# Kernel optimization log

Measured on AMD Instinct MI355X. Metric: run time of the kernel, lower is better.

The kernel has to match this reference:

```python
import jax, jax.numpy as jnp
import numpy as np

HEAD_DIM = 64  # hidden_dim 1024 // heads_num 16


def setup_inputs() -> dict:
    key = jax.random.key(0)
    ks = jax.random.split(key, 5)
    B, S, H = 2, 4096, 1024
    std = 1.0 / np.sqrt(H)
    return {
        "x": jax.random.normal(ks[0], (B, S, H), jnp.float32),
        "Wq": jax.random.normal(ks[1], (H, H), jnp.float32) * std,
        "bq": jnp.zeros((H,), jnp.float32),
        "Wk": jax.random.normal(ks[2], (H, H), jnp.float32) * std,
        "bk": jnp.zeros((H,), jnp.float32),
        "Wv": jax.random.normal(ks[3], (H, H), jnp.float32) * std,
        "bv": jnp.zeros((H,), jnp.float32),
        "Wo": jax.random.normal(ks[4], (H, H), jnp.float32) * std,
        "bo": jnp.zeros((H,), jnp.float32),
    }


def reference(x, Wq, bq, Wk, bk, Wv, bv, Wo, bo):
    # Linear projections (torch Linear: x @ W^T + b)
    q = jnp.einsum("bsh,oh->bso", x, Wq) + bq
    k = jnp.einsum("bsh,oh->bso", x, Wk) + bk
    v = jnp.einsum("bsh,oh->bso", x, Wv) + bv
    # all_to_all is identity on a single device (world size 1)
    scale = jnp.float32(HEAD_DIM) ** 0.5
    # Faithful to source: attention over the FULL hidden dim (no head split),
    # full [B, S, S] score matrix.
    scores = jnp.einsum("bqh,bkh->bqk", q, k) / scale
    weights = jax.nn.softmax(scores, axis=-1)
    attn = jnp.einsum("bqk,bkh->bqh", weights, v)
    out = jnp.einsum("bsh,oh->bso", attn, Wo) + bo
    return out
```

## Files before the change

### kernel.cpp

```cpp
#include <hip/hip_runtime.h>
#include <stdint.h>


typedef __bf16 bf16x8 __attribute__((ext_vector_type(8)));
typedef float  f32x4  __attribute__((ext_vector_type(4)));

__device__ __forceinline__ unsigned short f32_to_bf16_rne(float f) {
    uint32_t u = __builtin_bit_cast(uint32_t, f);
    uint32_t r = (u + 0x7FFFu + ((u >> 16) & 1u)) >> 16;
    return (unsigned short)r;
}

__global__ __launch_bounds__(256) void cvt_f32_bf16(
    const float* __restrict__ x, unsigned short* __restrict__ y, int n)
{
    int i = (blockIdx.x * 256 + threadIdx.x) * 4;
    if (i < n) {
        float4 v = *(const float4*)(x + i);
        ushort4 o;
        o.x = f32_to_bf16_rne(v.x);
        o.y = f32_to_bf16_rne(v.y);
        o.z = f32_to_bf16_rne(v.z);
        o.w = f32_to_bf16_rne(v.w);
        *(ushort4*)(y + i) = o;
    }
}

__global__ __launch_bounds__(256) void cvt_weights(
    const float* __restrict__ w0, const float* __restrict__ w1,
    const float* __restrict__ w2, const float* __restrict__ w3,
    unsigned short* __restrict__ dst, float* __restrict__ rsum)
{
    int b = blockIdx.x;
    if (b >= 4096) {
        int i = ((b - 4096) * 256 + threadIdx.x) * 4;
        *(float4*)(rsum + i) = float4{0.f, 0.f, 0.f, 0.f};
        return;
    }
    int which = b >> 10;
    const float* src = which == 0 ? w0 : which == 1 ? w1 : which == 2 ? w2 : w3;
    int i = ((b & 1023) * 256 + threadIdx.x) * 4;
    float4 v = *(const float4*)(src + i);
    ushort4 o;
    o.x = f32_to_bf16_rne(v.x);
    o.y = f32_to_bf16_rne(v.y);
    o.z = f32_to_bf16_rne(v.z);
    o.w = f32_to_bf16_rne(v.w);
    *(ushort4*)(dst + (size_t)which * 1048576 + i) = o;
}

#define BM 128
#define BN 128
#define BK 64

template <int MODE>
__global__ __launch_bounds__(256) void gemm_bt(
    const unsigned short* __restrict__ A,
    const unsigned short* __restrict__ Bt,
    void* __restrict__ C, void* __restrict__ C2,
    const float* __restrict__ b0, const float* __restrict__ b1,
    const float* __restrict__ b2, float* __restrict__ rowsum,
    float alpha, int M, int N, int K,
    long long aZ, long long bZ, long long cZ)
{
    __shared__ unsigned short ldsA[BM * BK];
    __shared__ unsigned short ldsB[BN * BK];

    int G  = gridDim.x * gridDim.y * gridDim.z;
    int l  = blockIdx.x + gridDim.x * (blockIdx.y + gridDim.y * blockIdx.z);
    int mb, nb, zb;
    if ((G & 7) == 0) {
        int perx = G >> 3;
        int idx  = (l & 7) * perx + (l >> 3);
        int NB = gridDim.x, Z = gridDim.z;
        mb = idx / (NB * Z);
        int rem = idx - mb * (NB * Z);
        zb = rem / NB;
        nb = rem - zb * NB;
    } else {
        mb = blockIdx.y; nb = blockIdx.x; zb = blockIdx.z;
    }

    const unsigned short* Ab = A  + (size_t)zb * aZ;
    const unsigned short* Bb = Bt + (size_t)zb * bZ;

    const int tid  = threadIdx.x;
    const int lane = tid & 63;
    const int wave = tid >> 6;
    const int quad = lane >> 4;
    const int l16  = lane & 15;
    const int wr   = wave >> 1;
    const int wc   = wave & 1;

    const int mBase = mb * BM;
    const int nBase = nb * BN;

    f32x4 acc[4][4] = {};

    for (int k0 = 0; k0 < K; k0 += BK) {
        #pragma unroll
        for (int i = 0; i < 4; ++i) {
            int base = (i * 4 + wave) * 64;
            int s    = base + lane;
            int row  = s >> 3;
            int col  = ((s ^ (s >> 3)) & 7) * 8;
            __builtin_amdgcn_global_load_lds(
                (const __attribute__((address_space(1))) void*)(Ab + (size_t)(mBase + row) * K + (size_t)(k0 + col)),
                (__attribute__((address_space(3))) void*)(&ldsA[base * 8]),
                16, 0, 0);
        }
        #pragma unroll
        for (int i = 0; i < 4; ++i) {
            int base = (i * 4 + wave) * 64;
            int s    = base + lane;
            int row  = s >> 3;
            int col  = ((s ^ (s >> 3)) & 7) * 8;
            __builtin_amdgcn_global_load_lds(
                (const __attribute__((address_space(1))) void*)(Bb + (size_t)(nBase + row) * K + (size_t)(k0 + col)),
                (__attribute__((address_space(3))) void*)(&ldsB[base * 8]),
                16, 0, 0);
        }
        __syncthreads();

        #pragma unroll
        for (int kk = 0; kk < 2; ++kk) {
            bf16x8 af[4], bfv[4];
            #pragma unroll
            for (int mi = 0; mi < 4; ++mi) {
                int r = wr * 64 + mi * 16 + l16;
                int c = kk * 4 + quad;
                af[mi] = *(const bf16x8*)(&ldsA[r * BK + (((c ^ r) & 7) << 3)]);
            }
            #pragma unroll
            for (int ni = 0; ni < 4; ++ni) {
                int r = wc * 64 + ni * 16 + l16;
                int c = kk * 4 + quad;
                bfv[ni] = *(const bf16x8*)(&ldsB[r * BK + (((c ^ r) & 7) << 3)]);
            }
            #pragma unroll
            for (int mi = 0; mi < 4; ++mi)
                #pragma unroll
                for (int ni = 0; ni < 4; ++ni)
                    acc[mi][ni] = __builtin_amdgcn_mfma_f32_16x16x32_bf16(
                        af[mi], bfv[ni], acc[mi][ni], 0, 0, 0);
        }
        __syncthreads();
    }

    if (MODE == 1) {
        unsigned short* Cz = (unsigned short*)C + (size_t)zb * cZ;
        #pragma unroll
        for (int mi = 0; mi < 4; ++mi)
            #pragma unroll
            for (int ni = 0; ni < 4; ++ni) {
                int col = nBase + wc * 64 + ni * 16 + l16;
                float b = b0 ? b0[col] : 0.f;
                #pragma unroll
                for (int r = 0; r < 4; ++r) {
                    int row = mBase + wr * 64 + mi * 16 + quad * 4 + r;
                    Cz[(size_t)row * N + col] = f32_to_bf16_rne(acc[mi][ni][r] + b);
                }
            }
    } else if (MODE == 3) {
        unsigned short* Pz = (unsigned short*)C + (size_t)zb * cZ;
        float* rs = rowsum + (size_t)zb * M;
        #pragma unroll
        for (int mi = 0; mi < 4; ++mi) {
            #pragma unroll
            for (int r = 0; r < 4; ++r) {
                int row = mBase + wr * 64 + mi * 16 + quad * 4 + r;
                float e[4];
                float partial = 0.f;
                #pragma unroll
                for (int ni = 0; ni < 4; ++ni) {
                    e[ni] = __expf(acc[mi][ni][r] * alpha);
                    partial += e[ni];
                }
                #pragma unroll
                for (int ni = 0; ni < 4; ++ni) {
                    int col = nBase + wc * 64 + ni * 16 + l16;
                    Pz[(size_t)row * N + col] = f32_to_bf16_rne(e[ni]);
                }
                #pragma unroll
                for (int off = 1; off < 16; off <<= 1)
                    partial += __shfl_xor(partial, off, 64);
                if (l16 == 0) atomicAdd(&rs[row], partial);
            }
        }
    } else if (MODE == 5) {
        const float* bias = (zb == 0) ? b0 : (zb == 1) ? b1 : b2;
        unsigned short* Cz = (zb < 2) ? ((unsigned short*)C + (size_t)zb * cZ)
                                      : (unsigned short*)C2;
        #pragma unroll
        for (int mi = 0; mi < 4; ++mi)
            #pragma unroll
            for (int ni = 0; ni < 4; ++ni) {
                int col = nBase + wc * 64 + ni * 16 + l16;
                float b = bias[col];
                #pragma unroll
                for (int r = 0; r < 4; ++r) {
                    int row = mBase + wr * 64 + mi * 16 + quad * 4 + r;
                    Cz[(size_t)row * N + col] = f32_to_bf16_rne(acc[mi][ni][r] + b);
                }
            }
    } else {
        float* Cz = (float*)C + (size_t)zb * cZ;
        const float* rs = rowsum + (size_t)zb * M;
        #pragma unroll
        for (int mi = 0; mi < 4; ++mi) {
            #pragma unroll
            for (int r = 0; r < 4; ++r) {
                int row = mBase + wr * 64 + mi * 16 + quad * 4 + r;
                float inv = 1.f / rs[row];
                #pragma unroll
                for (int ni = 0; ni < 4; ++ni) {
                    int col = nBase + wc * 64 + ni * 16 + l16;
                    Cz[(size_t)row * N + col] = acc[mi][ni][r] * inv + b0[col];
                }
            }
        }
    }
}

extern "C" void kernel_launch(void* const* d_in, const int* in_sizes, int n_in,
                              void* d_out, int out_size, void* d_ws, size_t ws_size,
                              hipStream_t stream)
{
    const float* x  = (const float*)d_in[0];
    const float* Wq = (const float*)d_in[1];
    const float* bq = (const float*)d_in[2];
    const float* Wk = (const float*)d_in[3];
    const float* bk = (const float*)d_in[4];
    const float* Wv = (const float*)d_in[5];
    const float* bv = (const float*)d_in[6];
    const float* Wo = (const float*)d_in[7];
    const float* bo = (const float*)d_in[8];
    float* out = (float*)d_out;

    const int Bsz = 2, S = 4096, H = 1024;
    const int M = Bsz * S;

    char* p = (char*)d_ws;
    auto alloc = [&](size_t bytes) -> char* {
        char* r = p; p += (bytes + 255) & ~(size_t)255; return r;
    };
    unsigned short* w16  = (unsigned short*)alloc((size_t)4 * H * H * 2);
    unsigned short* wq16 = w16;
    unsigned short* wo16 = w16 + (size_t)3 * H * H;
    unsigned short* q16  = (unsigned short*)alloc((size_t)M * H * 2);
    unsigned short* k16  = (unsigned short*)alloc((size_t)M * H * 2);
    unsigned short* vot16= (unsigned short*)alloc((size_t)Bsz * H * S * 2);
    float*          rsum = (float*)alloc((size_t)Bsz * S * 4);
    char* region = alloc((size_t)Bsz * S * S * 2);
    unsigned short* x16 = (unsigned short*)region;
    unsigned short* v16 = (unsigned short*)region + (size_t)M * H;
    unsigned short* p16 = (unsigned short*)region;

    cvt_f32_bf16<<<(M * H) / 1024, 256, 0, stream>>>(x, x16, M * H);
    cvt_weights<<<4096 + 8, 256, 0, stream>>>(Wq, Wk, Wv, Wo, w16, rsum);

    dim3 blk(256);

    gemm_bt<5><<<dim3(H / BN, M / BM, 3), blk, 0, stream>>>(
        x16, wq16, q16, v16, bq, bk, bv, nullptr, 1.f, M, H, H,
        0, (long long)H * H, (long long)M * H);

    gemm_bt<1><<<dim3(S / BN, H / BM, 2), blk, 0, stream>>>(
        wo16, v16, vot16, nullptr, nullptr, nullptr, nullptr, nullptr, 1.f,
        H, S, H, 0, (long long)S * H, (long long)H * S);

    gemm_bt<3><<<dim3(S / BN, S / BM, 2), blk, 0, stream>>>(
        q16, k16, p16, nullptr, nullptr, nullptr, nullptr, rsum, 0.125f,
        S, S, H, (long long)S * H, (long long)S * H, (long long)S * S);

    gemm_bt<6><<<dim3(H / BN, S / BM, 2), blk, 0, stream>>>(
        p16, vot16, out, nullptr, bo, nullptr, nullptr, rsum, 1.f,
        S, H, S, (long long)S * S, (long long)H * S, (long long)S * H);
}
```

Measured before the change: 387.0 us.

## Merge conversion kernels and fuse Wo·V and QK^T GEMMs into one launch

After: 386.0 us. No clear change (-0.3%).

```diff
diff --git a/kernel.cpp b/kernel.cpp
--- a/kernel.cpp
+++ b/kernel.cpp
@@ -11,75 +11,129 @@
     return (unsigned short)r;
 }
 
-__global__ __launch_bounds__(256) void cvt_f32_bf16(
-    const float* __restrict__ x, unsigned short* __restrict__ y, int n)
-{
-    int i = (blockIdx.x * 256 + threadIdx.x) * 4;
-    if (i < n) {
+#define BM 128
+#define BN 128
+#define BK 64
+
+__global__ __launch_bounds__(256) void cvt_all(
+    const float* __restrict__ x,
+    const float* __restrict__ w0, const float* __restrict__ w1,
+    const float* __restrict__ w2, const float* __restrict__ w3,
+    unsigned short* __restrict__ x16, unsigned short* __restrict__ w16,
+    float* __restrict__ rsum)
+{
+    int b = blockIdx.x;
+    if (b < 8192) {
+        int i = (b * 256 + threadIdx.x) * 4;
         float4 v = *(const float4*)(x + i);
         ushort4 o;
         o.x = f32_to_bf16_rne(v.x);
         o.y = f32_to_bf16_rne(v.y);
         o.z = f32_to_bf16_rne(v.z);
         o.w = f32_to_bf16_rne(v.w);
-        *(ushort4*)(y + i) = o;
-    }
-}
-
-__global__ __launch_bounds__(256) void cvt_weights(
-    const float* __restrict__ w0, const float* __restrict__ w1,
-    const float* __restrict__ w2, const float* __restrict__ w3,
-    unsigned short* __restrict__ dst, float* __restrict__ rsum)
-{
-    int b = blockIdx.x;
-    if (b >= 4096) {
-        int i = ((b - 4096) * 256 + threadIdx.x) * 4;
+        *(ushort4*)(x16 + i) = o;
+    } else if (b < 8192 + 4096) {
+        int bb = b - 8192;
+        int which = bb >> 10;
+        const float* src = which == 0 ? w0 : which == 1 ? w1 : which == 2 ? w2 : w3;
+        int i = ((bb & 1023) * 256 + threadIdx.x) * 4;
+        float4 v = *(const float4*)(src + i);
+        ushort4 o;
+        o.x = f32_to_bf16_rne(v.x);
+        o.y = f32_to_bf16_rne(v.y);
+        o.z = f32_to_bf16_rne(v.z);
+        o.w = f32_to_bf16_rne(v.w);
+        *(ushort4*)(w16 + (size_t)which * 1048576 + i) = o;
+    } else {
+        int i = ((b - 8192 - 4096) * 256 + threadIdx.x) * 4;
         *(float4*)(rsum + i) = float4{0.f, 0.f, 0.f, 0.f};
-        return;
-    }
-    int which = b >> 10;
-    const float* src = which == 0 ? w0 : which == 1 ? w1 : which == 2 ? w2 : w3;
-    int i = ((b & 1023) * 256 + threadIdx.x) * 4;
-    float4 v = *(const float4*)(src + i);
-    ushort4 o;
-    o.x = f32_to_bf16_rne(v.x);
-    o.y = f32_to_bf16_rne(v.y);
-    o.z = f32_to_bf16_rne(v.z);
-    o.w = f32_to_bf16_rne(v.w);
-    *(ushort4*)(dst + (size_t)which * 1048576 + i) = o;
-}
-
-#define BM 128
-#define BN 128
-#define BK 64
-
-template <int MODE>
+    }
+}
+
+template <int KC>
+__device__ __forceinline__ void gemm_core(
+    const unsigned short* __restrict__ Ab,
+    const unsigned short* __restrict__ Bb,
+    unsigned short* ldsA, unsigned short* ldsB,
+    int mBase, int nBase, int lane, int wave, f32x4 (&acc)[4][4])
+{
+    const int quad = lane >> 4;
+    const int l16  = lane & 15;
+    const int wr   = wave >> 1;
+    const int wc   = wave & 1;
+
+    for (int k0 = 0; k0 < KC; k0 += BK) {
+        #pragma unroll
+        for (int i = 0; i < 4; ++i) {
+            int base = (i * 4 + wave) * 64;
+            int s    = base + lane;
+            int row  = s >> 3;
+            int col  = ((s ^ (s >> 3)) & 7) * 8;
+            __builtin_amdgcn_global_load_lds(
+                (const __attribute__((address_space(1))) void*)(Ab + (size_t)(mBase + row) * KC + (size_t)(k0 + col)),
+                (__attribute__((address_space(3))) void*)(&ldsA[base * 8]),
+                16, 0, 0);
+        }
+        #pragma unroll
+        for (int i = 0; i < 4; ++i) {
+            int base = (i * 4 + wave) * 64;
+            int s    = base + lane;
+            int row  = s >> 3;
+            int col  = ((s ^ (s >> 3)) & 7) * 8;
+            __builtin_amdgcn_global_load_lds(
+                (const __attribute__((address_space(1))) void*)(Bb + (size_t)(nBase + row) * KC + (size_t)(k0 + col)),
+                (__attribute__((address_space(3))) void*)(&ldsB[base * 8]),
+                16, 0, 0);
+        }
+        __syncthreads();
+
+        #pragma unroll
+        for (int kk = 0; kk < 2; ++kk) {
+            bf16x8 af[4], bfv[4];
+            #pragma unroll
+            for (int mi = 0; mi < 4; ++mi) {
+                int r = wr * 64 + mi * 16 + l16;
+                int c = kk * 4 + quad;
+                af[mi] = *(const bf16x8*)(&ldsA[r * BK + (((c ^ r) & 7) << 3)]);
+            }
+            #pragma unroll
+            for (int ni = 0; ni < 4; ++ni) {
+                int r = wc * 64 + ni * 16 + l16;
+                int c = kk * 4 + quad;
+                bfv[ni] = *(const bf16x8*)(&ldsB[r * BK + (((c ^ r) & 7) << 3)]);
+            }
+            #pragma unroll
+            for (int mi = 0; mi < 4; ++mi)
+                #pragma unroll
+                for (int ni = 0; ni < 4; ++ni)
+                    acc[mi][ni] = __builtin_amdgcn_mfma_f32_16x16x32_bf16(
+                        af[mi], bfv[ni], acc[mi][ni], 0, 0, 0);
+        }
+        __syncthreads();
+    }
+}
+
+template <int MODE, int KC>
 __global__ __launch_bounds__(256) void gemm_bt(
     const unsigned short* __restrict__ A,
     const unsigned short* __restrict__ Bt,
     void* __restrict__ C, void* __restrict__ C2,
     const float* __restrict__ b0, const float* __restrict__ b1,
-    const float* __restrict__ b2, float* __restrict__ rowsum,
-    float alpha, int M, int N, int K,
-    long long aZ, long long bZ, long long cZ)
+    const float* __restrict__ b2, const float* __restrict__ rowsum,
+    int M, int N, long long aZ, long long bZ, long long cZ)
 {
     __shared__ unsigned short ldsA[BM * BK];
     __shared__ unsigned short ldsB[BN * BK];
 
     int G  = gridDim.x * gridDim.y * gridDim.z;
     int l  = blockIdx.x + gridDim.x * (blockIdx.y + gridDim.y * blockIdx.z);
-    int mb, nb, zb;
-    if ((G & 7) == 0) {
-        int perx = G >> 3;
-        int idx  = (l & 7) * perx + (l >> 3);
-        int NB = gridDim.x, Z = gridDim.z;
-        mb = idx / (NB * Z);
-        int rem = idx - mb * (NB * Z);
-        zb = rem / NB;
-        nb = rem - zb * NB;
-    } else {
-        mb = blockIdx.y; nb = blockIdx.x; zb = blockIdx.z;
-    }
+    int perx = G >> 3;
+    int idx  = (l & 7) * perx + (l >> 3);
+    int NB = gridDim.x, Z = gridDim.z;
+    int mb = idx / (NB * Z);
+    int rem = idx - mb * (NB * Z);
+    int zb = rem / NB;
+    int nb = rem - zb * NB;
 
     const unsigned short* Ab = A  + (size_t)zb * aZ;
     const unsigned short* Bb = Bt + (size_t)zb * bZ;
@@ -91,79 +145,102 @@
     const int l16  = lane & 15;
     const int wr   = wave >> 1;
     const int wc   = wave & 1;
-
     const int mBase = mb * BM;
     const int nBase = nb * BN;
 
     f32x4 acc[4][4] = {};
-
-    for (int k0 = 0; k0 < K; k0 += BK) {
-        #pragma unroll
-        for (int i = 0; i < 4; ++i) {
-            int base = (i * 4 + wave) * 64;
-            int s    = base + lane;
-            int row  = s >> 3;
-            int col  = ((s ^ (s >> 3)) & 7) * 8;
-            __builtin_amdgcn_global_load_lds(
-                (const __attribute__((address_space(1))) void*)(Ab + (size_t)(mBase + row) * K + (size_t)(k0 + col)),
-                (__attribute__((address_space(3))) void*)(&ldsA[base * 8]),
-                16, 0, 0);
-        }
-        #pragma unroll
-        for (int i = 0; i < 4; ++i) {
-            int base = (i * 4 + wave) * 64;
-            int s    = base + lane;
-            int row  = s >> 3;
-            int col  = ((s ^ (s >> 3)) & 7) * 8;
-            __builtin_amdgcn_global_load_lds(
-                (const __attribute__((address_space(1))) void*)(Bb + (size_t)(nBase + row) * K + (size_t)(k0 + col)),
-                (__attribute__((address_space(3))) void*)(&ldsB[base * 8]),
-                16, 0, 0);
-        }
-        __syncthreads();
-
-        #pragma unroll
-        for (int kk = 0; kk < 2; ++kk) {
-            bf16x8 af[4], bfv[4];
-            #pragma unroll
-            for (int mi = 0; mi < 4; ++mi) {
-                int r = wr * 64 + mi * 16 + l16;
-                int c = kk * 4 + quad;
-                af[mi] = *(const bf16x8*)(&ldsA[r * BK + (((c ^ r) & 7) << 3)]);
-            }
-            #pragma unroll
-            for (int ni = 0; ni < 4; ++ni) {
-                int r = wc * 64 + ni * 16 + l16;
-                int c = kk * 4 + quad;
-                bfv[ni] = *(const bf16x8*)(&ldsB[r * BK + (((c ^ r) & 7) << 3)]);
-            }
-            #pragma unroll
-            for (int mi = 0; mi < 4; ++mi)
-                #pragma unroll
-                for (int ni = 0; ni < 4; ++ni)
-                    acc[mi][ni] = __builtin_amdgcn_mfma_f32_16x16x32_bf16(
-                        af[mi], bfv[ni], acc[mi][ni], 0, 0, 0);
-        }
-        __syncthreads();
-    }
-
-    if (MODE == 1) {
-        unsigned short* Cz = (unsigned short*)C + (size_t)zb * cZ;
+    gemm_core<KC>(Ab, Bb, ldsA, ldsB, mBase, nBase, lane, wave, acc);
+
+    if (MODE == 5) {
+        const float* bias = (zb == 0) ? b0 : (zb == 1) ? b1 : b2;
+        unsigned short* Cz = (zb < 2) ? ((unsigned short*)C + (size_t)zb * cZ)
+                                      : (unsigned short*)C2;
         #pragma unroll
         for (int mi = 0; mi < 4; ++mi)
             #pragma unroll
             for (int ni = 0; ni < 4; ++ni) {
                 int col = nBase + wc * 64 + ni * 16 + l16;
-                float b = b0 ? b0[col] : 0.f;
+                float b = bias[col];
                 #pragma unroll
                 for (int r = 0; r < 4; ++r) {
                     int row = mBase + wr * 64 + mi * 16 + quad * 4 + r;
                     Cz[(size_t)row * N + col] = f32_to_bf16_rne(acc[mi][ni][r] + b);
                 }
             }
-    } else if (MODE == 3) {
-        unsigned short* Pz = (unsigned short*)C + (size_t)zb * cZ;
-        float* rs = rowsum + (size_t)zb * M;
+    } else {
+        float* Cz = (float*)C + (size_t)zb * cZ;
+        const float* rs = rowsum + (size_t)zb * M;
+        #pragma unroll
+        for (int mi = 0; mi < 4; ++mi) {
+            #pragma unroll
+            for (int r = 0; r < 4; ++r) {
+                int row = mBase + wr * 64 + mi * 16 + quad * 4 + r;
+                float inv = 1.f / rs[row];
+                #pragma unroll
+                for (int ni = 0; ni < 4; ++ni) {
+                    int col = nBase + wc * 64 + ni * 16 + l16;
+                    Cz[(size_t)row * N + col] = acc[mi][ni][r] * inv + b0[col];
+                }
+            }
+        }
+    }
+}
+
+__global__ __launch_bounds__(256) void gemm_dual(
+    const unsigned short* __restrict__ wo,
+    const unsigned short* __restrict__ v16,
+    unsigned short* __restrict__ vot16,
+    const unsigned short* __restrict__ q16,
+    const unsigned short* __restrict__ k16,
+    unsigned short* __restrict__ p16,
+    float* __restrict__ rowsum)
+{
+    __shared__ unsigned short ldsA[BM * BK];
+    __shared__ unsigned short ldsB[BN * BK];
+
+    const int S = 4096, H = 1024;
+    const long long SH = (long long)S * H;
+
+    int l   = blockIdx.x;
+    int idx = (l & 7) * 320 + (l >> 3);
+
+    const unsigned short* Ab;
+    const unsigned short* Bb;
+    unsigned short* Cb;
+    float* rs = nullptr;
+    int mBase, nBase;
+    bool isScore;
+
+    if (idx < 512) {
+        int z = idx >> 8, m = (idx >> 5) & 7, n = idx & 31;
+        Ab = wo;
+        Bb = v16 + (size_t)z * SH;
+        Cb = vot16 + (size_t)z * SH;
+        mBase = m * BM; nBase = n * BN;
+        isScore = false;
+    } else {
+        int sid = idx - 512;
+        int m = sid >> 6, z = (sid >> 5) & 1, n = sid & 31;
+        Ab = q16 + (size_t)z * SH;
+        Bb = k16 + (size_t)z * SH;
+        Cb = p16 + (size_t)z * S * S;
+        rs = rowsum + (size_t)z * S;
+        mBase = m * BM; nBase = n * BN;
+        isScore = true;
+    }
+
+    const int tid  = threadIdx.x;
+    const int lane = tid & 63;
+    const int wave = tid >> 6;
+    const int quad = lane >> 4;
+    const int l16  = lane & 15;
+    const int wr   = wave >> 1;
+    const int wc   = wave & 1;
+
+    f32x4 acc[4][4] = {};
+    gemm_core<1024>(Ab, Bb, ldsA, ldsB, mBase, nBase, lane, wave, acc);
+
+    if (isScore) {
         #pragma unroll
         for (int mi = 0; mi < 4; ++mi) {
             #pragma unroll
@@ -173,13 +250,13 @@
                 float partial = 0.f;
                 #pragma unroll
                 for (int ni = 0; ni < 4; ++ni) {
-                    e[ni] = __expf(acc[mi][ni][r] * alpha);
+                    e[ni] = __expf(acc[mi][ni][r] * 0.125f);
                     partial += e[ni];
                 }
                 #pragma unroll
                 for (int ni = 0; ni < 4; ++ni) {
                     int col = nBase + wc * 64 + ni * 16 + l16;
-                    Pz[(size_t)row * N + col] = f32_to_bf16_rne(e[ni]);
+                    Cb[(size_t)row * 4096 + col] = f32_to_bf16_rne(e[ni]);
                 }
                 #pragma unroll
                 for (int off = 1; off < 16; off <<= 1)
@@ -187,38 +264,18 @@
                 if (l16 == 0) atomicAdd(&rs[row], partial);
             }
         }
-    } else if (MODE == 5) {
-        const float* bias = (zb == 0) ? b0 : (zb == 1) ? b1 : b2;
-        unsigned short* Cz = (zb < 2) ? ((unsigned short*)C + (size_t)zb * cZ)
-                                      : (unsigned short*)C2;
+    } else {
         #pragma unroll
         for (int mi = 0; mi < 4; ++mi)
             #pragma unroll
             for (int ni = 0; ni < 4; ++ni) {
                 int col = nBase + wc * 64 + ni * 16 + l16;
-                float b = bias[col];
                 #pragma unroll
                 for (int r = 0; r < 4; ++r) {
                     int row = mBase + wr * 64 + mi * 16 + quad * 4 + r;
-                    Cz[(size_t)row * N + col] = f32_to_bf16_rne(acc[mi][ni][r] + b);
-                }
-            }
-    } else {
-        float* Cz = (float*)C + (size_t)zb * cZ;
-        const float* rs = rowsum + (size_t)zb * M;
-        #pragma unroll
-        for (int mi = 0; mi < 4; ++mi) {
-            #pragma unroll
-            for (int r = 0; r < 4; ++r) {
-                int row = mBase + wr * 64 + mi * 16 + quad * 4 + r;
-                float inv = 1.f / rs[row];
-                #pragma unroll
-                for (int ni = 0; ni < 4; ++ni) {
-                    int col = nBase + wc * 64 + ni * 16 + l16;
-                    Cz[(size_t)row * N + col] = acc[mi][ni][r] * inv + b0[col];
-                }
-            }
-        }
+                    Cb[(size_t)row * 4096 + col] = f32_to_bf16_rne(acc[mi][ni][r]);
+                }
+            }
     }
 }
 
@@ -249,31 +306,22 @@
     unsigned short* wo16 = w16 + (size_t)3 * H * H;
     unsigned short* q16  = (unsigned short*)alloc((size_t)M * H * 2);
     unsigned short* k16  = (unsigned short*)alloc((size_t)M * H * 2);
+    unsigned short* v16  = (unsigned short*)alloc((size_t)M * H * 2);
     unsigned short* vot16= (unsigned short*)alloc((size_t)Bsz * H * S * 2);
     float*          rsum = (float*)alloc((size_t)Bsz * S * 4);
     char* region = alloc((size_t)Bsz * S * S * 2);
     unsigned short* x16 = (unsigned short*)region;
-    unsigned short* v16 = (unsigned short*)region + (size_t)M * H;
     unsigned short* p16 = (unsigned short*)region;
 
-    cvt_f32_bf16<<<(M * H) / 1024, 256, 0, stream>>>(x, x16, M * H);
-    cvt_weights<<<4096 + 8, 256, 0, stream>>>(Wq, Wk, Wv, Wo, w16, rsum);
-
-    dim3 blk(256);
-
-    gemm_bt<5><<<dim3(H / BN, M / BM, 3), blk, 0, stream>>>(
-        x16, wq16, q16, v16, bq, bk, bv, nullptr, 1.f, M, H, H,
+    cvt_all<<<8192 + 4096 + 8, 256, 0, stream>>>(x, Wq, Wk, Wv, Wo, x16, w16, rsum);
+
+    gemm_bt<5, 1024><<<dim3(H / BN, M / BM, 3), 256, 0, stream>>>(
+        x16, wq16, q16, v16, bq, bk, bv, nullptr, M, H,
         0, (long long)H * H, (long long)M * H);
 
-    gemm_bt<1><<<dim3(S / BN, H / BM, 2), blk, 0, stream>>>(
-        wo16, v16, vot16, nullptr, nullptr, nullptr, nullptr, nullptr, 1.f,
-        H, S, H, 0, (long long)S * H, (long long)H * S);
-
-    gemm_bt<3><<<dim3(S / BN, S / BM, 2), blk, 0, stream>>>(
-        q16, k16, p16, nullptr, nullptr, nullptr, nullptr, rsum, 0.125f,
-        S, S, H, (long long)S * H, (long long)S * H, (long long)S * S);
-
-    gemm_bt<6><<<dim3(H / BN, S / BM, 2), blk, 0, stream>>>(
-        p16, vot16, out, nullptr, bo, nullptr, nullptr, rsum, 1.f,
-        S, H, S, (long long)S * S, (long long)H * S, (long long)S * H);
-}
+    gemm_dual<<<2560, 256, 0, stream>>>(wo16, v16, vot16, q16, k16, p16, rsum);
+
+    gemm_bt<6, 4096><<<dim3(H / BN, S / BM, 2), 256, 0, stream>>>(
+        p16, vot16, out, nullptr, bo, nullptr, nullptr, rsum, S, H,
+        (long long)S * S, (long long)H * S, (long long)S * H);
+}
```
